# Performance work log

Measured on AMD Instinct MI355X. Metric: run time of the kernel, lower is better.

Reference implementation:

```python
import jax, jax.numpy as jnp
import numpy as np

N_NODES = 50000


def _gcn_layer(x, src, dst, deg_inv_sqrt, W, b):
    # GCNConv (PyG defaults): h = x @ W; out = D^-1/2 (A+I) D^-1/2 h + b
    h = x @ W
    norm = deg_inv_sqrt[src] * deg_inv_sqrt[dst]          # [E]
    msg = h[src] * norm[:, None]                           # [E, d_out]
    agg = jax.ops.segment_sum(msg, dst, num_segments=N_NODES)
    agg = agg + h * (deg_inv_sqrt * deg_inv_sqrt)[:, None]  # self-loop term
    return agg + b


def _stack(x, src, dst, dis, W1, b1, W2, b2, W3, b3):
    h = jax.nn.relu(_gcn_layer(x, src, dst, dis, W1, b1))
    h = jax.nn.relu(_gcn_layer(h, src, dst, dis, W2, b2))
    return jax.nn.relu(_gcn_layer(h, src, dst, dis, W3, b3))


def setup_inputs() -> dict:
    key = jax.random.key(0)
    ks = jax.random.split(key, 16)
    din, lat, E = 128, 64, 800000
    x = jax.random.normal(ks[0], (N_NODES, din), dtype=jnp.float32)
    edge_index = jax.random.randint(ks[1], (2, E), 0, N_NODES, dtype=jnp.int64)

    def lin(k, fan_in, fan_out):
        s = 1.0 / np.sqrt(fan_in)
        kw, kb = jax.random.split(k)
        W = jax.random.uniform(kw, (fan_in, fan_out), minval=-s, maxval=s, dtype=jnp.float32)
        b = jax.random.uniform(kb, (fan_out,), minval=-s, maxval=s, dtype=jnp.float32)
        return W, b

    Wm1, bm1 = lin(ks[2], din, 64)
    Wm2, bm2 = lin(ks[3], 64, 128)
    Wm3, bm3 = lin(ks[4], 128, lat)
    Wl1, bl1 = lin(ks[5], din, 64)
    Wl2, bl2 = lin(ks[6], 64, 128)
    Wl3, bl3 = lin(ks[7], 128, lat)
    return {"x": x, "edge_index": edge_index,
            "Wm1": Wm1, "bm1": bm1, "Wm2": Wm2, "bm2": bm2, "Wm3": Wm3, "bm3": bm3,
            "Wl1": Wl1, "bl1": bl1, "Wl2": Wl2, "bl2": bl2, "Wl3": Wl3, "bl3": bl3}


def reference(x, edge_index, Wm1, bm1, Wm2, bm2, Wm3, bm3, Wl1, bl1, Wl2, bl2, Wl3, bl3):
    src, dst = edge_index[0], edge_index[1]
    # degree with self-loops (PyG: deg over dst of A+I)
    deg = jax.ops.segment_sum(jnp.ones_like(dst, dtype=x.dtype), dst, num_segments=N_NODES) + 1.0
    dis = jax.lax.rsqrt(deg)
    mu = _stack(x, src, dst, dis, Wm1, bm1, Wm2, bm2, Wm3, bm3)
    log = _stack(x, src, dst, dis, Wl1, bl1, Wl2, bl2, Wl3, bl3)
    return (mu, log)
```

## Files before the change

kernel.cpp:

```cpp
#include <hip/hip_runtime.h>

#define N_NODES_C 50000

__global__ void detect_kernel(const int* __restrict__ w, int ncheck, int* __restrict__ flag) {
    int tid = blockIdx.x * blockDim.x + threadIdx.x;
    if (tid < ncheck) {
        if (w[2 * tid + 1] != 0) *flag = 0;
    }
}

__global__ void count_kernel(const int* __restrict__ ei, int E, const int* __restrict__ flag,
                             int* __restrict__ counts) {
    int e = blockIdx.x * blockDim.x + threadIdx.x;
    if (e >= E) return;
    int shift = (*flag != 0) ? 1 : 0;
    int d = ei[(unsigned)(E + e) << shift];
    atomicAdd(&counts[d], 1);
}

__global__ void scan_kernel(const int* __restrict__ counts, int* __restrict__ row_start,
                            int* __restrict__ cursor, float* __restrict__ dis, int n) {
    __shared__ int wsum[16];
    __shared__ int carry;
    __shared__ int chunk_total;
    int tid = threadIdx.x;
    int lane = tid & 63;
    int wid = tid >> 6;
    if (tid == 0) carry = 0;
    __syncthreads();
    for (int base = 0; base < n; base += 1024) {
        int i = base + tid;
        int v = (i < n) ? counts[i] : 0;
        int x = v;
        #pragma unroll
        for (int off = 1; off < 64; off <<= 1) {
            int y = __shfl_up(x, off);
            if (lane >= off) x += y;
        }
        if (lane == 63) wsum[wid] = x;
        __syncthreads();
        if (tid == 0) {
            int run = 0;
            #pragma unroll
            for (int q = 0; q < 16; q++) { int t = wsum[q]; wsum[q] = run; run += t; }
            chunk_total = run;
        }
        __syncthreads();
        int excl = x - v + wsum[wid] + carry;
        if (i < n) {
            row_start[i] = excl;
            cursor[i] = excl;
            dis[i] = rsqrtf((float)v + 1.0f);
        }
        __syncthreads();
        if (tid == 0) carry += chunk_total;
        __syncthreads();
    }
    if (tid == 0) row_start[n] = carry;
}

__global__ void fill_kernel(const int* __restrict__ ei, int E, const int* __restrict__ flag,
                            int* __restrict__ cursor, int* __restrict__ csr_src) {
    int e = blockIdx.x * blockDim.x + threadIdx.x;
    if (e >= E) return;
    int shift = (*flag != 0) ? 1 : 0;
    int s = ei[(unsigned)e << shift];
    int d = ei[(unsigned)(E + e) << shift];
    int pos = atomicAdd(&cursor[d], 1);
    csr_src[pos] = s;
}

template <bool FINAL>
__global__ __launch_bounds__(256) void agg128_kernel(const float* __restrict__ h,
                                                     const int* __restrict__ row_start,
                                                     const int* __restrict__ csr_src,
                                                     const float* __restrict__ dis,
                                                     const float* __restrict__ bmu,
                                                     const float* __restrict__ blog,
                                                     float* __restrict__ out,
                                                     float* __restrict__ outlog, int M) {
    int wid = threadIdx.x >> 6;
    int lane = threadIdx.x & 63;
    int node = blockIdx.x * 4 + wid;
    if (node >= M) return;
    int half = lane >> 5;
    int c0 = (lane & 31) * 4;

    int s = row_start[node];
    int e = row_start[node + 1];
    float dn = dis[node];

    float a0 = 0.f, a1 = 0.f, a2 = 0.f, a3 = 0.f;
    int i = s + half;
    for (; i + 6 < e; i += 8) {
        int s0 = csr_src[i];
        int s1 = csr_src[i + 2];
        int s2 = csr_src[i + 4];
        int s3 = csr_src[i + 6];
        float w0 = dis[s0] * dn;
        float w1 = dis[s1] * dn;
        float w2 = dis[s2] * dn;
        float w3 = dis[s3] * dn;
        float4 v0 = *(const float4*)&h[(size_t)s0 * 128 + c0];
        float4 v1 = *(const float4*)&h[(size_t)s1 * 128 + c0];
        float4 v2 = *(const float4*)&h[(size_t)s2 * 128 + c0];
        float4 v3 = *(const float4*)&h[(size_t)s3 * 128 + c0];
        a0 = fmaf(w0, v0.x, a0); a1 = fmaf(w0, v0.y, a1);
        a2 = fmaf(w0, v0.z, a2); a3 = fmaf(w0, v0.w, a3);
        a0 = fmaf(w1, v1.x, a0); a1 = fmaf(w1, v1.y, a1);
        a2 = fmaf(w1, v1.z, a2); a3 = fmaf(w1, v1.w, a3);
        a0 = fmaf(w2, v2.x, a0); a1 = fmaf(w2, v2.y, a1);
        a2 = fmaf(w2, v2.z, a2); a3 = fmaf(w2, v2.w, a3);
        a0 = fmaf(w3, v3.x, a0); a1 = fmaf(w3, v3.y, a1);
        a2 = fmaf(w3, v3.z, a2); a3 = fmaf(w3, v3.w, a3);
    }
    for (; i < e; i += 2) {
        int s0 = csr_src[i];
        float w0 = dis[s0] * dn;
        float4 v0 = *(const float4*)&h[(size_t)s0 * 128 + c0];
        a0 = fmaf(w0, v0.x, a0); a1 = fmaf(w0, v0.y, a1);
        a2 = fmaf(w0, v0.z, a2); a3 = fmaf(w0, v0.w, a3);
    }
    a0 += __shfl_xor(a0, 32);
    a1 += __shfl_xor(a1, 32);
    a2 += __shfl_xor(a2, 32);
    a3 += __shfl_xor(a3, 32);

    float sw = dn * dn;
    float4 sv = *(const float4*)&h[(size_t)node * 128 + c0];
    a0 = fmaf(sw, sv.x, a0); a1 = fmaf(sw, sv.y, a1);
    a2 = fmaf(sw, sv.z, a2); a3 = fmaf(sw, sv.w, a3);

    if (half == 0) {
        if constexpr (FINAL) {
            float b0, b1, b2, b3;
            float* yp;
            if (c0 < 64) {
                b0 = bmu[c0]; b1 = bmu[c0 + 1]; b2 = bmu[c0 + 2]; b3 = bmu[c0 + 3];
                yp = out + (size_t)node * 64 + c0;
            } else {
                int c = c0 - 64;
                b0 = blog[c]; b1 = blog[c + 1]; b2 = blog[c + 2]; b3 = blog[c + 3];
                yp = outlog + (size_t)node * 64 + c;
            }
            float4 o;
            o.x = fmaxf(a0 + b0, 0.f);
            o.y = fmaxf(a1 + b1, 0.f);
            o.z = fmaxf(a2 + b2, 0.f);
            o.w = fmaxf(a3 + b3, 0.f);
            *(float4*)yp = o;
        } else {
            *(float4*)&out[(size_t)node * 128 + c0] = make_float4(a0, a1, a2, a3);
        }
    }
}

template <int K, int N, int LDXS, int XA, int XB, int BM, int KCH, int NT,
          bool RELU, bool BIAS>
__global__ __launch_bounds__(NT) void gemm3_kernel(const float* __restrict__ X,
                                                   const float* __restrict__ Wa,
                                                   const float* __restrict__ Wb,
                                                   const float* __restrict__ ba,
                                                   const float* __restrict__ bb,
                                                   float* __restrict__ Y, int ldy, int M) {
    constexpr int NTX = N / 8;
    constexpr int NTY = NT / NTX;
    constexpr int RPT = BM / NTY;
    constexpr int XLD = LDXS + 4;
    constexpr int NH = N / 2;
    constexpr int WTS = KCH + 4;
    constexpr int TPB = NTX / 2;
    __shared__ alignas(16) float xs[BM * XLD];
    __shared__ alignas(16) float wst[N * WTS];

    int t = threadIdx.x;
    int row0 = blockIdx.x * BM;

    constexpr int KQ = LDXS / 4;
    for (int i = t; i < BM * KQ; i += NT) {
        int r = i / KQ, kq = i % KQ;
        float4 v = make_float4(0.f, 0.f, 0.f, 0.f);
        if (row0 + r < M) v = *(const float4*)&X[(size_t)(row0 + r) * LDXS + 4 * kq];
        *(float4*)&xs[r * XLD + 4 * kq] = v;
    }

    int tx = t % NTX;
    int ty = t / NTX;
    int branch = (tx >= TPB) ? 1 : 0;
    int txl = tx - branch * TPB;
    int xoff = branch ? XB : XA;
    int wbase = (branch * NH + txl) * WTS;

    float acc[RPT][8];
    #pragma unroll
    for (int rr = 0; rr < RPT; rr++)
        #pragma unroll
        for (int j = 0; j < 8; j++) acc[rr][j] = 0.f;

    for (int kc = 0; kc < K; kc += KCH) {
        __syncthreads();
        for (int i = t; i < KCH * N; i += NT) {
            int kk = i / N, c = i % N;
            float v = (c < NH) ? Wa[(size_t)(kc + kk) * NH + c]
                               : Wb[(size_t)(kc + kk) * NH + (c - NH)];
            wst[c * WTS + kk] = v;
        }
        __syncthreads();

        #pragma unroll
        for (int kk4 = 0; kk4 < KCH / 4; ++kk4) {
            float4 wv[8];
            #pragma unroll
            for (int j = 0; j < 8; j++)
                wv[j] = *(const float4*)&wst[wbase + j * (TPB * WTS) + 4 * kk4];
            #pragma unroll
            for (int rr = 0; rr < RPT; rr++) {
                float4 xv = *(const float4*)&xs[(ty * RPT + rr) * XLD + xoff + kc + 4 * kk4];
                #pragma unroll
                for (int j = 0; j < 8; j++) {
                    acc[rr][j] = fmaf(xv.x, wv[j].x, acc[rr][j]);
                    acc[rr][j] = fmaf(xv.y, wv[j].y, acc[rr][j]);
                    acc[rr][j] = fmaf(xv.z, wv[j].z, acc[rr][j]);
                    acc[rr][j] = fmaf(xv.w, wv[j].w, acc[rr][j]);
                }
            }
        }
    }

    float bj[8];
    #pragma unroll
    for (int j = 0; j < 8; j++) {
        if constexpr (BIAS) {
            const float* bp = branch ? bb : ba;
            bj[j] = bp[txl + j * TPB];
        } else {
            bj[j] = 0.f;
        }
    }
    #pragma unroll
    for (int rr = 0; rr < RPT; rr++) {
        int row = row0 + ty * RPT + rr;
        if (row < M) {
            float* yp = Y + (size_t)row * ldy + branch * NH + txl;
            #pragma unroll
            for (int j = 0; j < 8; j++) {
                float o = acc[rr][j] + bj[j];
                if constexpr (RELU) o = fmaxf(o, 0.f);
                yp[j * TPB] = o;
            }
        }
    }
}

extern "C" void kernel_launch(void* const* d_in, const int* in_sizes, int n_in,
                              void* d_out, int out_size, void* d_ws, size_t ws_size,
                              hipStream_t stream) {
    const float* x   = (const float*)d_in[0];
    const int*   ei  = (const int*)d_in[1];
    const float* Wm1 = (const float*)d_in[2];  const float* bm1 = (const float*)d_in[3];
    const float* Wm2 = (const float*)d_in[4];  const float* bm2 = (const float*)d_in[5];
    const float* Wm3 = (const float*)d_in[6];  const float* bm3 = (const float*)d_in[7];
    const float* Wl1 = (const float*)d_in[8];  const float* bl1 = (const float*)d_in[9];
    const float* Wl2 = (const float*)d_in[10]; const float* bl2 = (const float*)d_in[11];
    const float* Wl3 = (const float*)d_in[12]; const float* bl3 = (const float*)d_in[13];
    float* out = (float*)d_out;

    const int M = N_NODES_C;
    const int E = in_sizes[1] / 2;

    char* ws = (char*)d_ws;
    size_t off = 0;
    auto alloc = [&](size_t bytes) {
        size_t o = off;
        off += (bytes + 255) & ~(size_t)255;
        return o;
    };
    int*   flag      = (int*)(ws + alloc(4));
    int*   counts    = (int*)(ws + alloc((size_t)M * 4));
    int*   row_start = (int*)(ws + alloc((size_t)(M + 1) * 4));
    int*   cursor    = (int*)(ws + alloc((size_t)M * 4));
    float* dis       = (float*)(ws + alloc((size_t)M * 4));
    int*   csr_src   = (int*)(ws + alloc((size_t)E * 4));
    float* bufA      = (float*)(ws + alloc((size_t)M * 256 * 4));
    float* bufB      = (float*)(ws + alloc((size_t)M * 256 * 4));

    hipMemsetAsync(flag, 1, 4, stream);
    hipMemsetAsync(counts, 0, (size_t)M * 4, stream);

    int ncheck = (E < 2048) ? E : 2048;
    detect_kernel<<<(ncheck + 255) / 256, 256, 0, stream>>>(ei, ncheck, flag);
    count_kernel<<<(E + 255) / 256, 256, 0, stream>>>(ei, E, flag, counts);
    scan_kernel<<<1, 1024, 0, stream>>>(counts, row_start, cursor, dis, M);
    fill_kernel<<<(E + 255) / 256, 256, 0, stream>>>(ei, E, flag, cursor, csr_src);

    int ablocks = (M + 3) / 4;

    agg128_kernel<false><<<ablocks, 256, 0, stream>>>(x, row_start, csr_src, dis,
                                                      nullptr, nullptr, bufA, nullptr, M);

    gemm3_kernel<128, 128, 128, 0, 0, 64, 32, 256, true, true>
        <<<(M + 63) / 64, 256, 0, stream>>>(bufA, Wm1, Wl1, bm1, bl1, bufB, 128, M);

    agg128_kernel<false><<<ablocks, 256, 0, stream>>>(bufB, row_start, csr_src, dis,
                                                      nullptr, nullptr, bufA, nullptr, M);

    gemm3_kernel<64, 256, 128, 0, 64, 64, 16, 256, true, true>
        <<<(M + 63) / 64, 256, 0, stream>>>(bufA, Wm2, Wl2, bm2, bl2, bufB, 256, M);

    gemm3_kernel<128, 128, 256, 0, 128, 32, 32, 128, false, false>
        <<<(M + 31) / 32, 128, 0, stream>>>(bufB, Wm3, Wl3, nullptr, nullptr, bufA, 128, M);

    agg128_kernel<true><<<ablocks, 256, 0, stream>>>(bufA, row_start, csr_src, dis,
                                                     bm3, bl3, out, out + (size_t)M * 64, M);
}
```

Baseline: 569.7 us.

## Rewrite dense GEMM with K-chunked X staging, row-strided 8x8 micro-tiles and larger blocks

Replaces gemm3 with gemm4. The new kernel stages X per K-chunk into shared memory, where the old one loaded whole rows up front, and stores W k-major. Threads now own rows strided by NTY with scalar broadcast reads instead of float4 reads. Block tiles grow to 128 rows for layers 1 and 3, which means fewer blocks and more reuse of W but less occupancy and possibly more LDS bank conflicts. A SHARED mode avoids duplicating X when both branches read the same columns.

```diff
diff --git a/kernel.cpp b/kernel.cpp
--- a/kernel.cpp
+++ b/kernel.cpp
@@ -155,9 +155,9 @@
     }
 }
 
-template <int K, int N, int LDXS, int XA, int XB, int BM, int KCH, int NT,
+template <int K, int LDX, int XA, int XB, int N, int BM, int KCH, int NT,
           bool RELU, bool BIAS>
-__global__ __launch_bounds__(NT) void gemm3_kernel(const float* __restrict__ X,
+__global__ __launch_bounds__(NT) void gemm4_kernel(const float* __restrict__ X,
                                                    const float* __restrict__ Wa,
                                                    const float* __restrict__ Wb,
                                                    const float* __restrict__ ba,
@@ -166,30 +166,31 @@
     constexpr int NTX = N / 8;
     constexpr int NTY = NT / NTX;
     constexpr int RPT = BM / NTY;
-    constexpr int XLD = LDXS + 4;
     constexpr int NH = N / 2;
-    constexpr int WTS = KCH + 4;
+    constexpr bool SHARED = (XA == XB);
+    constexpr int NS = SHARED ? 1 : 2;
+    constexpr int RS = NS * KCH + 1;
     constexpr int TPB = NTX / 2;
-    __shared__ alignas(16) float xs[BM * XLD];
-    __shared__ alignas(16) float wst[N * WTS];
+    static_assert(RPT == 8, "micro-tile must be 8x8");
+
+    __shared__ float xs[BM * RS];
+    __shared__ float ws[KCH * N];
 
     int t = threadIdx.x;
     int row0 = blockIdx.x * BM;
-
-    constexpr int KQ = LDXS / 4;
-    for (int i = t; i < BM * KQ; i += NT) {
-        int r = i / KQ, kq = i % KQ;
-        float4 v = make_float4(0.f, 0.f, 0.f, 0.f);
-        if (row0 + r < M) v = *(const float4*)&X[(size_t)(row0 + r) * LDXS + 4 * kq];
-        *(float4*)&xs[r * XLD + 4 * kq] = v;
-    }
-
     int tx = t % NTX;
     int ty = t / NTX;
-    int branch = (tx >= TPB) ? 1 : 0;
-    int txl = tx - branch * TPB;
-    int xoff = branch ? XB : XA;
-    int wbase = (branch * NH + txl) * WTS;
+
+    int cb, cst, xslot;
+    if constexpr (SHARED) {
+        cb = tx; cst = NTX; xslot = 0;
+    } else {
+        int branch = tx / TPB;
+        int txl = tx - branch * TPB;
+        cb = branch * NH + txl;
+        cst = TPB;
+        xslot = branch;
+    }
 
     float acc[RPT][8];
     #pragma unroll
@@ -199,31 +200,36 @@
 
     for (int kc = 0; kc < K; kc += KCH) {
         __syncthreads();
+        for (int i = t; i < BM * NS * KCH; i += NT) {
+            int r = i / (NS * KCH), cc = i % (NS * KCH);
+            int slot = cc / KCH, kk = cc - slot * KCH;
+            int gcol = (slot ? XB : XA) + kc + kk;
+            int row = row0 + r;
+            float v = (row < M) ? X[(size_t)row * LDX + gcol] : 0.f;
+            xs[r * RS + cc] = v;
+        }
         for (int i = t; i < KCH * N; i += NT) {
-            int kk = i / N, c = i % N;
+            int kk = i / N, c = i - kk * N;
             float v = (c < NH) ? Wa[(size_t)(kc + kk) * NH + c]
                                : Wb[(size_t)(kc + kk) * NH + (c - NH)];
-            wst[c * WTS + kk] = v;
-        }
-        __syncthreads();
-
-        #pragma unroll
-        for (int kk4 = 0; kk4 < KCH / 4; ++kk4) {
-            float4 wv[8];
-            #pragma unroll
-            for (int j = 0; j < 8; j++)
-                wv[j] = *(const float4*)&wst[wbase + j * (TPB * WTS) + 4 * kk4];
-            #pragma unroll
-            for (int rr = 0; rr < RPT; rr++) {
-                float4 xv = *(const float4*)&xs[(ty * RPT + rr) * XLD + xoff + kc + 4 * kk4];
+            ws[kk * N + c] = v;
+        }
+        __syncthreads();
+
+        #pragma unroll 2
+        for (int kk = 0; kk < KCH; ++kk) {
+            float wv[8];
+            #pragma unroll
+            for (int j = 0; j < 8; j++) wv[j] = ws[kk * N + cb + j * cst];
+            float xv[RPT];
+            #pragma unroll
+            for (int rr = 0; rr < RPT; rr++)
+                xv[rr] = xs[(ty + rr * NTY) * RS + xslot * KCH + kk];
+            #pragma unroll
+            for (int rr = 0; rr < RPT; rr++)
                 #pragma unroll
-                for (int j = 0; j < 8; j++) {
-                    acc[rr][j] = fmaf(xv.x, wv[j].x, acc[rr][j]);
-                    acc[rr][j] = fmaf(xv.y, wv[j].y, acc[rr][j]);
-                    acc[rr][j] = fmaf(xv.z, wv[j].z, acc[rr][j]);
-                    acc[rr][j] = fmaf(xv.w, wv[j].w, acc[rr][j]);
-                }
-            }
+                for (int j = 0; j < 8; j++)
+                    acc[rr][j] = fmaf(xv[rr], wv[j], acc[rr][j]);
         }
     }
 
@@ -231,22 +237,22 @@
     #pragma unroll
     for (int j = 0; j < 8; j++) {
         if constexpr (BIAS) {
-            const float* bp = branch ? bb : ba;
-            bj[j] = bp[txl + j * TPB];
+            int c = cb + j * cst;
+            bj[j] = (c < NH) ? ba[c] : bb[c - NH];
         } else {
             bj[j] = 0.f;
         }
     }
     #pragma unroll
     for (int rr = 0; rr < RPT; rr++) {
-        int row = row0 + ty * RPT + rr;
+        int row = row0 + ty + rr * NTY;
         if (row < M) {
-            float* yp = Y + (size_t)row * ldy + branch * NH + txl;
+            float* yp = Y + (size_t)row * ldy;
             #pragma unroll
             for (int j = 0; j < 8; j++) {
                 float o = acc[rr][j] + bj[j];
                 if constexpr (RELU) o = fmaxf(o, 0.f);
-                yp[j * TPB] = o;
+                yp[cb + j * cst] = o;
             }
         }
     }
@@ -298,17 +304,17 @@
     agg128_kernel<false><<<ablocks, 256, 0, stream>>>(x, row_start, csr_src, dis,
                                                       nullptr, nullptr, bufA, nullptr, M);
 
-    gemm3_kernel<128, 128, 128, 0, 0, 64, 32, 256, true, true>
-        <<<(M + 63) / 64, 256, 0, stream>>>(bufA, Wm1, Wl1, bm1, bl1, bufB, 128, M);
+    gemm4_kernel<128, 128, 0, 0, 128, 128, 32, 256, true, true>
+        <<<(M + 127) / 128, 256, 0, stream>>>(bufA, Wm1, Wl1, bm1, bl1, bufB, 128, M);
 
     agg128_kernel<false><<<ablocks, 256, 0, stream>>>(bufB, row_start, csr_src, dis,
                                                       nullptr, nullptr, bufA, nullptr, M);
 
-    gemm3_kernel<64, 256, 128, 0, 64, 64, 16, 256, true, true>
+    gemm4_kernel<64, 128, 0, 64, 256, 64, 32, 256, true, true>
         <<<(M + 63) / 64, 256, 0, stream>>>(bufA, Wm2, Wl2, bm2, bl2, bufB, 256, M);
 
-    gemm3_kernel<128, 128, 256, 0, 128, 32, 32, 128, false, false>
-        <<<(M + 31) / 32, 128, 0, stream>>>(bufB, Wm3, Wl3, nullptr, nullptr, bufA, 128, M);
+    gemm4_kernel<128, 256, 0, 128, 128, 128, 32, 256, false, false>
+        <<<(M + 127) / 128, 256, 0, stream>>>(bufB, Wm3, Wl3, nullptr, nullptr, bufA, 128, M);
 
     agg128_kernel<true><<<ablocks, 256, 0, stream>>>(bufA, row_start, csr_src, dis,
                                                      bm3, bl3, out, out + (size_t)M * 64, M);
```

Result: slower. 590.1 us (+3.6%).
